# Optimization experiments

Measured on AMD Instinct MI355X. Metric: run time of the kernel, lower is better.

The kernel has to match this reference:

```python
import jax, jax.numpy as jnp
import numpy as np

G = 64          # grid_size
BC = 16         # base_channels
LATENT = 128

def _conv3d_s2(x, w, b):
    # x: [B,C,D,H,W], w: [O,I,3,3,3], stride 2, pad 1
    y = jax.lax.conv_general_dilated(
        x, w, window_strides=(2, 2, 2), padding=((1, 1), (1, 1), (1, 1)),
        dimension_numbers=('NCDHW', 'OIDHW', 'NCDHW'))
    return y + b[None, :, None, None, None]

def setup_inputs() -> dict:
    key = jax.random.key(0)
    ks = jax.random.split(key, 9)
    B, N = 32, 16384
    partial_coords = jax.random.uniform(ks[0], (B, N, 3), jnp.float32, -1.0, 1.0)
    def he(k, shape, fan_in):
        return jax.random.normal(k, shape, jnp.float32) * np.float32(np.sqrt(2.0 / fan_in))
    w1 = he(ks[1], (BC, 1, 3, 3, 3), 1 * 27)
    b1 = jnp.zeros((BC,), jnp.float32)
    w2 = he(ks[2], (2 * BC, BC, 3, 3, 3), BC * 27)
    b2 = jnp.zeros((2 * BC,), jnp.float32)
    w3 = he(ks[3], (4 * BC, 2 * BC, 3, 3, 3), 2 * BC * 27)
    b3 = jnp.zeros((4 * BC,), jnp.float32)
    fc_in = 4 * BC * (G // 8) ** 3
    fc_w = he(ks[4], (LATENT, fc_in), fc_in)
    fc_b = jnp.zeros((LATENT,), jnp.float32)
    return {'partial_coords': partial_coords, 'w1': w1, 'b1': b1, 'w2': w2,
            'b2': b2, 'w3': w3, 'b3': b3, 'fc_w': fc_w, 'fc_b': fc_b}

def reference(partial_coords, w1, b1, w2, b2, w3, b3, fc_w, fc_b):
    B, N, _ = partial_coords.shape
    # voxelize: scale [-1,1] -> [0, G-1], truncate (matches torch .long()), clamp
    coords_scaled = (partial_coords + 1.0) * 0.5 * (G - 1)
    ci = jnp.clip(coords_scaled.astype(jnp.int32), 0, G - 1)  # [B,N,3] = (x,y,z)
    bidx = jnp.broadcast_to(jnp.arange(B, dtype=jnp.int32)[:, None], (B, N))
    grid = jnp.zeros((B, G, G, G), jnp.float32)
    # grid[b, z, y, x] = 1.0  (single vectorized scatter)
    grid = grid.at[bidx, ci[..., 2], ci[..., 1], ci[..., 0]].set(1.0)
    x = grid[:, None]  # [B,1,G,G,G]
    x = jax.nn.relu(_conv3d_s2(x, w1, b1))
    x = jax.nn.relu(_conv3d_s2(x, w2, b2))
    x = jax.nn.relu(_conv3d_s2(x, w3, b3))  # [B,4*BC,G/8,G/8,G/8]
    feat = x.reshape(B, -1)
    return feat @ fc_w.T + fc_b  # [B,128]
```

## Files before the change

### kernel.cpp

```cpp
#include <hip/hip_runtime.h>
#include <hip/hip_bf16.h>


typedef __attribute__((ext_vector_type(8))) short bf16x8;
typedef __attribute__((ext_vector_type(4))) float f32x4;

__device__ inline unsigned short f2bf(float f) {
    __hip_bfloat16 h = __float2bfloat16(f);
    return *reinterpret_cast<unsigned short*>(&h);
}

__global__ void k_scatter_wtrans(const float* __restrict__ coords,
                                 unsigned char* __restrict__ grid,
                                 const float* __restrict__ w2,
                                 unsigned short* __restrict__ w2b,
                                 const float* __restrict__ w3,
                                 unsigned short* __restrict__ w3b) {
    int blk = blockIdx.x;
    if (blk < 2048) {
        int i = blk * 256 + threadIdx.x;
        float cx = coords[3 * i + 0];
        float cy = coords[3 * i + 1];
        float cz = coords[3 * i + 2];
        int ix = (int)((cx + 1.0f) * 0.5f * 63.0f);
        int iy = (int)((cy + 1.0f) * 0.5f * 63.0f);
        int iz = (int)((cz + 1.0f) * 0.5f * 63.0f);
        ix = min(max(ix, 0), 63);
        iy = min(max(iy, 0), 63);
        iz = min(max(iz, 0), 63);
        int b = i >> 14;
        grid[((b * 64 + iz) * 64 + iy) * 64 + ix] = 1;
    } else {
        int i = (blk - 2048) * 256 + threadIdx.x;
        if (i < 14336) {
            int sh = i >> 9, oc = (i >> 4) & 31, c = i & 15;
            float v = (sh < 27) ? w2[oc * 432 + c * 27 + sh] : 0.0f;
            w2b[i] = f2bf(v);
        } else {
            int j = i - 14336;
            if (j < 55296) {
                int sh = j >> 11, oc = (j >> 5) & 63, c = j & 31;
                w3b[j] = f2bf(w3[oc * 864 + c * 27 + sh]);
            }
        }
    }
}

__global__ __launch_bounds__(256) void k_conv1(
        const unsigned char* __restrict__ grid,
        const float* __restrict__ w1,
        const float* __restrict__ b1,
        unsigned short* __restrict__ c1b) {
    __shared__ float hal[9 * 17 * 20];
    const int t = threadIdx.x;
    const int blk = blockIdx.x;
    const int b = blk >> 7;
    const int zb = (blk >> 4) & 7;
    const int yb = (blk >> 2) & 3;
    const int xb = blk & 3;
    const int iz0 = 8 * zb - 1, iy0 = 16 * yb - 1, ix0 = 16 * xb - 1;

    const unsigned char* g = grid + b * 262144;
    for (int i = t; i < 2601; i += 256) {
        int hz = i / 289, rm = i - hz * 289;
        int hy = rm / 17, hx = rm - hy * 17;
        int iz = iz0 + hz, iy = iy0 + hy, ix = ix0 + hx;
        bool ok = (iz >= 0) & (iy >= 0) & (ix >= 0);
        float v = ok ? (float)g[(iz * 64 + iy) * 64 + ix] : 0.0f;
        int ux = (hx & 1) ? 10 + (hx >> 1) : (hx >> 1);
        hal[(hz * 17 + hy) * 20 + ux] = v;
    }
    __syncthreads();

    const int x = t & 7, y = (t >> 3) & 7, tz = t >> 6;
    const int base = (2 * tz * 17) * 20 + (2 * y) * 20 + x;
    float in27[27];
#pragma unroll
    for (int kz = 0; kz < 3; ++kz)
#pragma unroll
        for (int ky = 0; ky < 3; ++ky)
#pragma unroll
            for (int kx = 0; kx < 3; ++kx) {
                int uxo = (kx == 1) ? 10 : ((kx == 2) ? 1 : 0);
                in27[kz * 9 + ky * 3 + kx] =
                    hal[base + (kz * 17 + ky) * 20 + uxo];
            }
    float r[16];
#pragma unroll
    for (int oc = 0; oc < 16; ++oc) {
        float acc = b1[oc];
#pragma unroll
        for (int k = 0; k < 27; ++k) acc = fmaf(w1[oc * 27 + k], in27[k], acc);
        r[oc] = fmaxf(acc, 0.0f);
    }
    unsigned int dw[8];
#pragma unroll
    for (int j = 0; j < 8; ++j)
        dw[j] = (unsigned int)f2bf(r[2 * j]) | ((unsigned int)f2bf(r[2 * j + 1]) << 16);
    int oz = 4 * zb + tz, oy = 8 * yb + y, ox = 8 * xb + x;
    size_t idx = ((size_t)(b * 32 + oz) * 32 + oy) * 32 + ox;
    char* base_o = (char*)c1b + idx * 32;
    *(int4*)base_o        = int4{(int)dw[0], (int)dw[1], (int)dw[2], (int)dw[3]};
    *(int4*)(base_o + 16) = int4{(int)dw[4], (int)dw[5], (int)dw[6], (int)dw[7]};
}

__device__ constexpr int abase2(int sh) {
    return (sh / 9) * 18480 + (((sh % 9) / 3) & 1) * 9520 +
           (((sh % 9) / 3) >> 1) * 560 + (sh % 3) * 32;
}

__global__ __launch_bounds__(512, 4) void k_conv2_mfma(
        const unsigned short* __restrict__ c1b,
        const unsigned short* __restrict__ w2b,
        const float* __restrict__ b2,
        unsigned short* __restrict__ c2b) {
    __shared__ __align__(16) char smem[55440];
    const int t = threadIdx.x;
    const int b = blockIdx.x >> 5;
    const int zo = (blockIdx.x >> 1) & 15;
    const int xh = blockIdx.x & 1;
    const int lane = t & 63;
    const int wid = t >> 6;

    const char* src = (const char*)c1b + (size_t)b * (32768 * 32);
    for (int i = t; i < 1683; i += 512) {
        int kz = i / 561, rem = i - kz * 561;
        int iy_st = rem / 17, c = rem - iy_st * 17;
        int iz = 2 * zo + kz - 1;
        int iy = iy_st - 1;
        int ix = (xh << 4) + c - 1;
        int4 v0 = {0, 0, 0, 0}, v1 = {0, 0, 0, 0};
        if ((iz >= 0) & (iy >= 0) & (ix >= 0)) {
            const char* gp = src + ((size_t)((iz * 32 + iy) * 32 + ix)) * 32;
            v0 = *(const int4*)gp;
            v1 = *(const int4*)(gp + 16);
        }
        char* d = smem + kz * 18480 + (iy_st & 1) * 9520 + (iy_st >> 1) * 560 + c * 32;
        *(int4*)d = v0;
        *(int4*)(d + 16) = v1;
    }
    __syncthreads();

    const int y16 = lane & 15;
    const int g = lane >> 4;
    const int h = g & 1;
    const int s = g >> 1;
    const int laneA = y16 * 560 + h * 16;
    const int laneB = (lane & 15) * 32 + h * 16 + s * 1024;
    const int xl64 = wid * 64;
    const char* wbase = (const char*)w2b;

    f32x4 acc0 = {0, 0, 0, 0}, acc1 = {0, 0, 0, 0};

#pragma unroll
    for (int sp = 0; sp < 14; ++sp) {
        const int sh0 = 2 * sp;
        const int sh1 = (2 * sp + 1 < 27) ? 2 * sp + 1 : 26;
        const int a0 = abase2(sh0);
        const int d01 = abase2(sh1) - a0;
        bf16x8 A = *(const bf16x8*)(smem + laneA + a0 + (s ? d01 : 0) + xl64);
        const char* wb = wbase + sp * 2048 + laneB;
        bf16x8 B0 = *(const bf16x8*)wb;
        bf16x8 B1 = *(const bf16x8*)(wb + 512);
        acc0 = __builtin_amdgcn_mfma_f32_16x16x32_bf16(A, B0, acc0, 0, 0, 0);
        acc1 = __builtin_amdgcn_mfma_f32_16x16x32_bf16(A, B1, acc1, 0, 0, 0);
    }

    __syncthreads();
    float* sOut = (float*)smem;
    {
        int ocl = lane & 15;
        int yb = (lane >> 4) * 4;
#pragma unroll
        for (int r = 0; r < 4; ++r) {
            sOut[ocl * 129        + (yb + r) * 8 + wid] = acc0[r];
            sOut[(ocl + 16) * 129 + (yb + r) * 8 + wid] = acc1[r];
        }
    }
    __syncthreads();
    {
        int vox = t >> 2, q = t & 3;
        unsigned int dw[4];
#pragma unroll
        for (int j = 0; j < 4; ++j) {
            int oc0 = 8 * q + 2 * j;
            float v0 = fmaxf(sOut[oc0 * 129 + vox] + b2[oc0], 0.0f);
            float v1 = fmaxf(sOut[(oc0 + 1) * 129 + vox] + b2[oc0 + 1], 0.0f);
            dw[j] = (unsigned int)f2bf(v0) | ((unsigned int)f2bf(v1) << 16);
        }
        char* dst = (char*)c2b +
                    ((size_t)b * 4096 + zo * 256 + (vox >> 3) * 16 + xh * 8 + (vox & 7)) * 64 +
                    q * 16;
        *(int4*)dst = int4{(int)dw[0], (int)dw[1], (int)dw[2], (int)dw[3]};
    }
}

__global__ __launch_bounds__(512) void k_conv3_mfma(
        const unsigned short* __restrict__ c2b,
        const unsigned short* __restrict__ w3b,
        const float* __restrict__ b3,
        float* __restrict__ feat) {
    __shared__ __align__(16) char smem[55488];
    const int t = threadIdx.x;
    const int b = blockIdx.x >> 3;
    const int zo = blockIdx.x & 7;
    const int lane = t & 63;
    const int wid = t >> 6;

    if (t < 396) {
        int p3 = t / 132, j = t % 132;
        int v = j >> 2, g = j & 3;
        int iy_st = (v < 17) ? 0 : (v - 16);
        int ix_st = (v < 17) ? v : 0;
        int ux = (ix_st & 1) ? 9 + (ix_st >> 1) : (ix_st >> 1);
        int u = (p3 * 17 + iy_st) * 17 + ux;
        *(int4*)(smem + u * 64 + g * 16) = int4{0, 0, 0, 0};
    }

    const char* src = (const char*)c2b + (size_t)b * 262144;
#pragma unroll
    for (int r = 0; r < 6; ++r) {
        int i = r * 512 + t;
        int g = i & 3, vox = i >> 2;
        int kz = vox >> 8, pos = vox & 255;
        int iy = pos >> 4, ix = pos & 15;
        int iz = 2 * zo + kz - 1;
        int4 v = {0, 0, 0, 0};
        if (iz >= 0)
            v = *(const int4*)(src + ((size_t)(iz * 256 + pos)) * 64 + g * 16);
        int ix_st = ix + 1;
        int ux = (ix_st & 1) ? 9 + (ix_st >> 1) : (ix_st >> 1);
        int u = (kz * 17 + iy + 1) * 17 + ux;
        *(int4*)(smem + u * 64 + g * 16) = v;
    }
    __syncthreads();

    const int mt = wid >> 1;
    const int ntp = wid & 1;
    const int m = mt * 16 + (lane & 15);
    const int y = m >> 3, x = m & 7;
    const int g = lane >> 4;
    const int laneA = (34 * y + x) * 64 + g * 16;
    const char* wb_base = (const char*)w3b + (ntp * 32 + (lane & 15)) * 64 + g * 16;

    f32x4 acc0 = {0, 0, 0, 0}, acc1 = {0, 0, 0, 0};

#pragma unroll
    for (int sh = 0; sh < 27; ++sh) {
        const int kz = sh / 9, ky = (sh % 9) / 3, kx = sh % 3;
        const int uxc = (kx == 0) ? 0 : ((kx == 1) ? 9 : 1);
        const int aoff = (289 * kz + 17 * ky + uxc) * 64;
        bf16x8 A = *(const bf16x8*)(smem + laneA + aoff);
        const char* wb = wb_base + sh * 4096;
        bf16x8 B0 = *(const bf16x8*)wb;
        bf16x8 B1 = *(const bf16x8*)(wb + 1024);
        acc0 = __builtin_amdgcn_mfma_f32_16x16x32_bf16(A, B0, acc0, 0, 0, 0);
        acc1 = __builtin_amdgcn_mfma_f32_16x16x32_bf16(A, B1, acc1, 0, 0, 0);
    }

    __syncthreads();
    float* sOut = (float*)smem;
    {
        int ocl = lane & 15;
        int mb = mt * 16 + (lane >> 4) * 4;
#pragma unroll
        for (int r = 0; r < 4; ++r) {
            sOut[(ntp * 32 + ocl) * 65 + mb + r]      = acc0[r];
            sOut[(ntp * 32 + 16 + ocl) * 65 + mb + r] = acc1[r];
        }
    }
    __syncthreads();
    {
        int oc = t >> 3, q = t & 7;
        float bb = b3[oc];
        float* dst = feat + (size_t)b * 32768 + oc * 512 + zo * 64 + q * 8;
#pragma unroll
        for (int k = 0; k < 8; ++k) {
            float v = sOut[oc * 65 + q * 8 + k] + bb;
            dst[k] = fmaxf(v, 0.0f);
        }
    }
}

__global__ void k_fc_partial(const float* __restrict__ feat,
                             const float* __restrict__ fc_w,
                             float* __restrict__ part) {
    __shared__ float lds[256 * 36];
    int fchunk = blockIdx.x & 127;
    int lg = blockIdx.x >> 7;
    int t = threadIdx.x;
    int f0 = fchunk * 256;
    for (int b = 0; b < 32; ++b)
        lds[t * 36 + b] = feat[b * 32768 + f0 + t];
    __syncthreads();

    int l = lg * 32 + (t >> 3);
    int bq = t & 7;
    const float* wrow = fc_w + l * 32768 + f0;
    float a0 = 0.f, a1 = 0.f, a2 = 0.f, a3 = 0.f;
    for (int f4 = 0; f4 < 64; ++f4) {
        float4 w4 = *(const float4*)(wrow + f4 * 4);
        const float* p = &lds[(f4 * 4) * 36 + bq * 4];
        a0 = fmaf(p[0], w4.x, a0); a1 = fmaf(p[1], w4.x, a1);
        a2 = fmaf(p[2], w4.x, a2); a3 = fmaf(p[3], w4.x, a3);
        p += 36;
        a0 = fmaf(p[0], w4.y, a0); a1 = fmaf(p[1], w4.y, a1);
        a2 = fmaf(p[2], w4.y, a2); a3 = fmaf(p[3], w4.y, a3);
        p += 36;
        a0 = fmaf(p[0], w4.z, a0); a1 = fmaf(p[1], w4.z, a1);
        a2 = fmaf(p[2], w4.z, a2); a3 = fmaf(p[3], w4.z, a3);
        p += 36;
        a0 = fmaf(p[0], w4.w, a0); a1 = fmaf(p[1], w4.w, a1);
        a2 = fmaf(p[2], w4.w, a2); a3 = fmaf(p[3], w4.w, a3);
    }
    int b0 = bq * 4;
    float* pd = part + (size_t)fchunk * 4096 + l;
    pd[(b0 + 0) * 128] = a0;
    pd[(b0 + 1) * 128] = a1;
    pd[(b0 + 2) * 128] = a2;
    pd[(b0 + 3) * 128] = a3;
}

__global__ void k_fc_reduce(const float* __restrict__ part,
                            const float* __restrict__ fc_b,
                            float* __restrict__ out) {
    int idx = blockIdx.x * 256 + threadIdx.x;
    int l = idx & 127;
    float s = fc_b[l];
#pragma unroll 8
    for (int fc = 0; fc < 128; ++fc)
        s += part[fc * 4096 + idx];
    out[idx] = s;
}

extern "C" void kernel_launch(void* const* d_in, const int* in_sizes, int n_in,
                              void* d_out, int out_size, void* d_ws, size_t ws_size,
                              hipStream_t stream) {
    const float* coords = (const float*)d_in[0];
    const float* w1 = (const float*)d_in[1];
    const float* b1 = (const float*)d_in[2];
    const float* w2 = (const float*)d_in[3];
    const float* b2 = (const float*)d_in[4];
    const float* w3 = (const float*)d_in[5];
    const float* b3 = (const float*)d_in[6];
    const float* fc_w = (const float*)d_in[7];
    const float* fc_b = (const float*)d_in[8];

    unsigned char* grid_u8 = (unsigned char*)d_ws;
    unsigned short* c1b = (unsigned short*)((char*)d_ws + 8388608);
    unsigned short* c2b = (unsigned short*)((char*)d_ws + 75497472);
    float* feat = (float*)((char*)d_ws + 92274688);
    float* part = (float*)((char*)d_ws + 96468992);
    unsigned short* w2b = (unsigned short*)((char*)d_ws + 98566144);
    unsigned short* w3b = (unsigned short*)((char*)d_ws + 98697216);
    float* out = (float*)d_out;

    hipMemsetAsync(grid_u8, 0, 8388608, stream);

    k_scatter_wtrans<<<2320, 256, 0, stream>>>(coords, grid_u8, w2, w2b, w3, w3b);
    k_conv1<<<4096, 256, 0, stream>>>(grid_u8, w1, b1, c1b);
    k_conv2_mfma<<<1024, 512, 0, stream>>>(c1b, w2b, b2, c2b);
    k_conv3_mfma<<<256, 512, 0, stream>>>(c2b, w3b, b3, feat);
    k_fc_partial<<<512, 256, 0, stream>>>(feat, fc_w, part);
    k_fc_reduce<<<16, 256, 0, stream>>>(part, fc_b, out);
}
```

Before: 163.6 us.

## Replace fp32 FC partial+reduce with bf16 MFMA kernel using atomic accumulation

Converts fc_w to bf16 inside the scatter/weight-transform kernel and has conv3 write bf16 features. The separate scalar-FMA partial and reduce kernels become a single MFMA kernel that atomically adds into a zeroed output. This aims to cut FC compute and memory traffic and remove one launch. The cost is an extra pass that reads all 16MB of fp32 fc_w every call, bf16 rounding of the FC operands, and nondeterministic atomic summation order.

```diff
diff --git a/kernel.cpp b/kernel.cpp
--- a/kernel.cpp
+++ b/kernel.cpp
@@ -15,7 +15,9 @@
                                  const float* __restrict__ w2,
                                  unsigned short* __restrict__ w2b,
                                  const float* __restrict__ w3,
-                                 unsigned short* __restrict__ w3b) {
+                                 unsigned short* __restrict__ w3b,
+                                 const float* __restrict__ fc_w,
+                                 unsigned short* __restrict__ fc_wb) {
     int blk = blockIdx.x;
     if (blk < 2048) {
         int i = blk * 256 + threadIdx.x;
@@ -30,7 +32,7 @@
         iz = min(max(iz, 0), 63);
         int b = i >> 14;
         grid[((b * 64 + iz) * 64 + iy) * 64 + ix] = 1;
-    } else {
+    } else if (blk < 2320) {
         int i = (blk - 2048) * 256 + threadIdx.x;
         if (i < 14336) {
             int sh = i >> 9, oc = (i >> 4) & 31, c = i & 15;
@@ -43,6 +45,17 @@
                 w3b[j] = f2bf(w3[oc * 864 + c * 27 + sh]);
             }
         }
+    } else {
+        int u = (blk - 2320) * 256 + threadIdx.x;
+        const float* src = fc_w + (size_t)u * 8;
+        float4 lo = *(const float4*)src;
+        float4 hi = *(const float4*)(src + 4);
+        unsigned int dw[4];
+        dw[0] = (unsigned int)f2bf(lo.x) | ((unsigned int)f2bf(lo.y) << 16);
+        dw[1] = (unsigned int)f2bf(lo.z) | ((unsigned int)f2bf(lo.w) << 16);
+        dw[2] = (unsigned int)f2bf(hi.x) | ((unsigned int)f2bf(hi.y) << 16);
+        dw[3] = (unsigned int)f2bf(hi.z) | ((unsigned int)f2bf(hi.w) << 16);
+        *(int4*)(fc_wb + (size_t)u * 8) = int4{(int)dw[0], (int)dw[1], (int)dw[2], (int)dw[3]};
     }
 }
 
@@ -199,7 +212,7 @@
         const unsigned short* __restrict__ c2b,
         const unsigned short* __restrict__ w3b,
         const float* __restrict__ b3,
-        float* __restrict__ feat) {
+        unsigned short* __restrict__ featb) {
     __shared__ __align__(16) char smem[55488];
     const int t = threadIdx.x;
     const int b = blockIdx.x >> 3;
@@ -273,64 +286,73 @@
     {
         int oc = t >> 3, q = t & 7;
         float bb = b3[oc];
-        float* dst = feat + (size_t)b * 32768 + oc * 512 + zo * 64 + q * 8;
-#pragma unroll
-        for (int k = 0; k < 8; ++k) {
-            float v = sOut[oc * 65 + q * 8 + k] + bb;
-            dst[k] = fmaxf(v, 0.0f);
-        }
-    }
-}
-
-__global__ void k_fc_partial(const float* __restrict__ feat,
-                             const float* __restrict__ fc_w,
-                             float* __restrict__ part) {
-    __shared__ float lds[256 * 36];
-    int fchunk = blockIdx.x & 127;
-    int lg = blockIdx.x >> 7;
-    int t = threadIdx.x;
-    int f0 = fchunk * 256;
-    for (int b = 0; b < 32; ++b)
-        lds[t * 36 + b] = feat[b * 32768 + f0 + t];
-    __syncthreads();
-
-    int l = lg * 32 + (t >> 3);
-    int bq = t & 7;
-    const float* wrow = fc_w + l * 32768 + f0;
-    float a0 = 0.f, a1 = 0.f, a2 = 0.f, a3 = 0.f;
-    for (int f4 = 0; f4 < 64; ++f4) {
-        float4 w4 = *(const float4*)(wrow + f4 * 4);
-        const float* p = &lds[(f4 * 4) * 36 + bq * 4];
-        a0 = fmaf(p[0], w4.x, a0); a1 = fmaf(p[1], w4.x, a1);
-        a2 = fmaf(p[2], w4.x, a2); a3 = fmaf(p[3], w4.x, a3);
-        p += 36;
-        a0 = fmaf(p[0], w4.y, a0); a1 = fmaf(p[1], w4.y, a1);
-        a2 = fmaf(p[2], w4.y, a2); a3 = fmaf(p[3], w4.y, a3);
-        p += 36;
-        a0 = fmaf(p[0], w4.z, a0); a1 = fmaf(p[1], w4.z, a1);
-        a2 = fmaf(p[2], w4.z, a2); a3 = fmaf(p[3], w4.z, a3);
-        p += 36;
-        a0 = fmaf(p[0], w4.w, a0); a1 = fmaf(p[1], w4.w, a1);
-        a2 = fmaf(p[2], w4.w, a2); a3 = fmaf(p[3], w4.w, a3);
-    }
-    int b0 = bq * 4;
-    float* pd = part + (size_t)fchunk * 4096 + l;
-    pd[(b0 + 0) * 128] = a0;
-    pd[(b0 + 1) * 128] = a1;
-    pd[(b0 + 2) * 128] = a2;
-    pd[(b0 + 3) * 128] = a3;
-}
-
-__global__ void k_fc_reduce(const float* __restrict__ part,
-                            const float* __restrict__ fc_b,
-                            float* __restrict__ out) {
-    int idx = blockIdx.x * 256 + threadIdx.x;
-    int l = idx & 127;
-    float s = fc_b[l];
-#pragma unroll 8
-    for (int fc = 0; fc < 128; ++fc)
-        s += part[fc * 4096 + idx];
-    out[idx] = s;
+        unsigned int dw[4];
+#pragma unroll
+        for (int j = 0; j < 4; ++j) {
+            float v0 = fmaxf(sOut[oc * 65 + q * 8 + 2 * j] + bb, 0.0f);
+            float v1 = fmaxf(sOut[oc * 65 + q * 8 + 2 * j + 1] + bb, 0.0f);
+            dw[j] = (unsigned int)f2bf(v0) | ((unsigned int)f2bf(v1) << 16);
+        }
+        char* dst = (char*)featb + (size_t)b * 65536 + oc * 1024 + zo * 128 + q * 16;
+        *(int4*)dst = int4{(int)dw[0], (int)dw[1], (int)dw[2], (int)dw[3]};
+    }
+}
+
+__global__ __launch_bounds__(256) void k_fc_mfma(
+        const unsigned short* __restrict__ featb,
+        const unsigned short* __restrict__ fc_wb,
+        const float* __restrict__ fc_b,
+        float* __restrict__ out) {
+    __shared__ __align__(16) char smem[32 * 272];
+    const int t = threadIdx.x;
+    const int blk = blockIdx.x;
+    const int f0 = blk << 7;
+
+    {
+        int b = t >> 3, seg = t & 7;
+        const char* gp = (const char*)featb + (size_t)b * 65536 + f0 * 2 + seg * 32;
+        char* d = smem + b * 272 + seg * 32;
+        *(int4*)d = *(const int4*)gp;
+        *(int4*)(d + 16) = *(const int4*)(gp + 16);
+    }
+    __syncthreads();
+
+    const int lane = t & 63;
+    const int w = t >> 6;
+    const int n = lane & 15;
+    const int g = lane >> 4;
+
+    f32x4 acc00 = {0, 0, 0, 0}, acc01 = {0, 0, 0, 0};
+    f32x4 acc10 = {0, 0, 0, 0}, acc11 = {0, 0, 0, 0};
+
+    const char* wb0 = (const char*)fc_wb + ((size_t)(2 * w * 16 + n)) * 65536 + f0 * 2 + g * 16;
+    const char* wb1 = wb0 + 16 * 65536;
+
+#pragma unroll
+    for (int ks = 0; ks < 4; ++ks) {
+        bf16x8 A0 = *(const bf16x8*)(smem + n * 272 + ks * 64 + g * 16);
+        bf16x8 A1 = *(const bf16x8*)(smem + (16 + n) * 272 + ks * 64 + g * 16);
+        bf16x8 B0 = *(const bf16x8*)(wb0 + ks * 64);
+        bf16x8 B1 = *(const bf16x8*)(wb1 + ks * 64);
+        acc00 = __builtin_amdgcn_mfma_f32_16x16x32_bf16(A0, B0, acc00, 0, 0, 0);
+        acc10 = __builtin_amdgcn_mfma_f32_16x16x32_bf16(A1, B0, acc10, 0, 0, 0);
+        acc01 = __builtin_amdgcn_mfma_f32_16x16x32_bf16(A0, B1, acc01, 0, 0, 0);
+        acc11 = __builtin_amdgcn_mfma_f32_16x16x32_bf16(A1, B1, acc11, 0, 0, 0);
+    }
+
+    const int bo = (lane >> 4) * 4;
+    const int l0 = 2 * w * 16 + (lane & 15);
+    const int l1 = l0 + 16;
+    const bool bias = (blk == 0);
+    const float bb0 = bias ? fc_b[l0] : 0.0f;
+    const float bb1 = bias ? fc_b[l1] : 0.0f;
+#pragma unroll
+    for (int r = 0; r < 4; ++r) {
+        atomicAdd(&out[(bo + r) * 128 + l0],      acc00[r] + bb0);
+        atomicAdd(&out[(bo + r + 16) * 128 + l0], acc10[r] + bb0);
+        atomicAdd(&out[(bo + r) * 128 + l1],      acc01[r] + bb1);
+        atomicAdd(&out[(bo + r + 16) * 128 + l1], acc11[r] + bb1);
+    }
 }
 
 extern "C" void kernel_launch(void* const* d_in, const int* in_sizes, int n_in,
@@ -349,18 +371,19 @@
     unsigned char* grid_u8 = (unsigned char*)d_ws;
     unsigned short* c1b = (unsigned short*)((char*)d_ws + 8388608);
     unsigned short* c2b = (unsigned short*)((char*)d_ws + 75497472);
-    float* feat = (float*)((char*)d_ws + 92274688);
-    float* part = (float*)((char*)d_ws + 96468992);
+    unsigned short* featb = (unsigned short*)((char*)d_ws + 92274688);
     unsigned short* w2b = (unsigned short*)((char*)d_ws + 98566144);
     unsigned short* w3b = (unsigned short*)((char*)d_ws + 98697216);
+    unsigned short* fc_wb = (unsigned short*)((char*)d_ws + 98807808);
     float* out = (float*)d_out;
 
     hipMemsetAsync(grid_u8, 0, 8388608, stream);
-
-    k_scatter_wtrans<<<2320, 256, 0, stream>>>(coords, grid_u8, w2, w2b, w3, w3b);
+    hipMemsetAsync(out, 0, 32 * 128 * sizeof(float), stream);
+
+    k_scatter_wtrans<<<4368, 256, 0, stream>>>(coords, grid_u8, w2, w2b, w3, w3b,
+                                               fc_w, fc_wb);
     k_conv1<<<4096, 256, 0, stream>>>(grid_u8, w1, b1, c1b);
     k_conv2_mfma<<<1024, 512, 0, stream>>>(c1b, w2b, b2, c2b);
-    k_conv3_mfma<<<256, 512, 0, stream>>>(c2b, w3b, b3, feat);
-    k_fc_partial<<<512, 256, 0, stream>>>(feat, fc_w, part);
-    k_fc_reduce<<<16, 256, 0, stream>>>(part, fc_b, out);
-}
+    k_conv3_mfma<<<256, 512, 0, stream>>>(c2b, w3b, b3, featb);
+    k_fc_mfma<<<256, 256, 0, stream>>>(featb, fc_wb, fc_b, out);
+}
```

Result: faster. 159.8 us (-2.3%).
